# Optimization experiments

Measured on AMD Instinct MI355X. Metric: run time of the kernel, lower is better.

Reference implementation:

```python
import jax, jax.numpy as jnp
import numpy as np

N_NODES = 50000
N_EDGES = 800000
F_IN, F_HID, F_OUT = 128, 256, 64


def setup_inputs() -> dict:
    key = jax.random.key(0)
    ks = jax.random.split(key, 8)
    return {
        "x": jax.random.normal(ks[0], (N_NODES, F_IN), dtype=jnp.float32),
        "edge_index": jax.random.randint(ks[1], (2, N_EDGES), 0, N_NODES, dtype=jnp.int32),
        "W_l1": jax.random.normal(ks[2], (F_IN, F_HID), dtype=jnp.float32) * (1.0 / np.sqrt(F_IN)),
        "W_r1": jax.random.normal(ks[3], (F_IN, F_HID), dtype=jnp.float32) * (1.0 / np.sqrt(F_IN)),
        "b1": jnp.zeros((F_HID,), dtype=jnp.float32),
        "W_l2": jax.random.normal(ks[4], (F_HID, F_OUT), dtype=jnp.float32) * (1.0 / np.sqrt(F_HID)),
        "W_r2": jax.random.normal(ks[5], (F_HID, F_OUT), dtype=jnp.float32) * (1.0 / np.sqrt(F_HID)),
        "b2": jnp.zeros((F_OUT,), dtype=jnp.float32),
    }


def _sage_conv(x, src, dst, W_l, W_r, b):
    # PyG SAGEConv, mean aggregation:
    #   out = mean_{j in N(i)} x_j @ W_l + b + x_i @ W_r
    n = x.shape[0]
    msgs = x[src]                                              # [E, F] gather
    agg_sum = jax.ops.segment_sum(msgs, dst, num_segments=n)   # [N, F] scatter-add
    deg = jax.ops.segment_sum(jnp.ones_like(dst, dtype=x.dtype), dst, num_segments=n)
    agg = agg_sum / jnp.maximum(deg, 1.0)[:, None]             # isolated nodes -> 0
    return agg @ W_l + x @ W_r + b


def reference(x, edge_index, W_l1, W_r1, b1, W_l2, W_r2, b2):
    src, dst = edge_index[0], edge_index[1]
    # layer 1 + relu (dropout is identity in eval mode)
    h = jax.nn.relu(_sage_conv(x, src, dst, W_l1, W_r1, b1))
    # layer 2, multi_class=False -> sigmoid
    out = jax.nn.sigmoid(_sage_conv(h, src, dst, W_l2, W_r2, b2))
    return out
```

## Files before the change

### kernel.cpp

```cpp
#include <hip/hip_runtime.h>
#include <cstdint>
#include <cstddef>


#define N_NODES 50000
#define N_EDGES 800000
#define F_IN 128
#define F_HID 256
#define F_OUT 64
#define CAP 64

#define NBIN ((N_NODES + 255) / 256)
#define EPB 4096
#define NBLK_A ((N_EDGES + EPB - 1) / EPB)
#define CHUNK 64

#define PREP_TOTAL (N_NODES * 64 + 256 * 256 + 128 * 256)
#define NBLK_PREP ((PREP_TOTAL + 255) / 256)

typedef __attribute__((ext_vector_type(8))) short bf16x8;
typedef __attribute__((ext_vector_type(4))) float f32x4;
typedef __attribute__((ext_vector_type(2))) float f32x2;

__device__ inline unsigned short f2bf(float f) {
    unsigned int u = __float_as_uint(f);
    u += 0x7fffu + ((u >> 16) & 1u);
    return (unsigned short)(u >> 16);
}
__device__ inline unsigned int pack_bf2(float lo, float hi) {
    return (unsigned int)f2bf(lo) | ((unsigned int)f2bf(hi) << 16);
}
__device__ inline float bf_lo(unsigned int u) { return __uint_as_float(u << 16); }
__device__ inline float bf_hi(unsigned int u) { return __uint_as_float(u & 0xffff0000u); }

__global__ __launch_bounds__(256) void binprep_kernel(
    const int* __restrict__ src, const int* __restrict__ dst, int* __restrict__ blkbincnt,
    unsigned int* __restrict__ chunks, const float* __restrict__ x,
    const float* __restrict__ Wl1, const float* __restrict__ Wr1, const float* __restrict__ Wl2,
    const float* __restrict__ Wr2, unsigned int* __restrict__ xbf,
    unsigned short* __restrict__ xq16, short* __restrict__ Bt1, short* __restrict__ Bt2) {
    __shared__ unsigned int ls[NBIN * CHUNK];
    __shared__ int hist[NBIN];
    const int bid = blockIdx.x;
    const int tid = threadIdx.x;
    if (bid < NBLK_A) {
        for (int i = tid; i < NBIN; i += 256) hist[i] = 0;
        __syncthreads();
        const int base = bid * EPB;
        const int nloc = min(EPB, N_EDGES - base);
        for (int j = tid; j < nloc; j += 256) {
            int e = base + j;
            int d = dst[e];
            int s = src[e];
            int bin = d >> 8;
            int p = atomicAdd(&hist[bin], 1);
            if (p < CHUNK) ls[bin * CHUNK + p] = ((unsigned int)(d & 255) << 16) | (unsigned int)s;
        }
        __syncthreads();
        for (int i = tid; i < NBIN; i += 256) blkbincnt[bid * NBIN + i] = hist[i];
        unsigned int* outp = &chunks[(size_t)bid * NBIN * CHUNK];
        for (int idx = tid; idx < NBIN * CHUNK; idx += 256) {
            int bin = idx >> 6, i = idx & 63;
            if (i < min(hist[bin], CHUNK)) outp[idx] = ls[idx];
        }
        return;
    }
    int i = (bid - NBLK_A) * 256 + tid;
    if (i < N_NODES * 64) {
        int row = i >> 6, c = i & 63;
        float2 f = *reinterpret_cast<const float2*>(&x[(size_t)row * F_IN + 2 * c]);
        xbf[(size_t)row * 64 + c] = pack_bf2(f.x, f.y);
        xq16[(size_t)row * 64 + c] =
            (unsigned short)(__builtin_amdgcn_cvt_pk_fp8_f32(f.x, f.y, 0, false) & 0xffff);
        return;
    }
    i -= N_NODES * 64;
    if (i < 256 * 256) {
        int k = i >> 8, n = i & 255;
        float v = (k < 128) ? Wl1[k * 256 + n] : Wr1[(k - 128) * 256 + n];
        Bt1[n * 256 + k] = (short)f2bf(v);
        return;
    }
    i -= 256 * 256;
    if (i < 128 * 256) {
        int k = i >> 7, n = i & 127;
        float v = (n < 64) ? Wl2[k * 64 + n] : Wr2[k * 64 + (n - 64)];
        Bt2[n * 256 + k] = (short)f2bf(v);
    }
}

__global__ __launch_bounds__(256) void binpartB_kernel(const unsigned int* __restrict__ chunks,
                                                       const int* __restrict__ blkbincnt,
                                                       int* __restrict__ cnt,
                                                       unsigned short* __restrict__ slots) {
    __shared__ int cur[256];
    __shared__ unsigned short ls[256 * CAP];
    __shared__ int ccnt[NBLK_A];
    const int bin = blockIdx.x;
    const int tid = threadIdx.x;
    cur[tid] = 0;
    for (int i = tid; i < NBLK_A; i += 256) ccnt[i] = min(blkbincnt[i * NBIN + bin], CHUNK);
    __syncthreads();
    for (int idx = tid; idx < NBLK_A * CHUNK; idx += 256) {
        int blk = idx >> 6, i = idx & 63;
        if (i < ccnt[blk]) {
            unsigned int pk = chunks[((size_t)blk * NBIN + bin) * CHUNK + i];
            int dl = pk >> 16;
            int p = atomicAdd(&cur[dl], 1);
            if (p < CAP) ls[dl * CAP + p] = (unsigned short)(pk & 0xffffu);
        }
    }
    __syncthreads();
    const int node = bin * 256 + tid;
    if (node < N_NODES) cnt[node] = cur[tid];
    const uint4* lsv = reinterpret_cast<const uint4*>(ls);
    uint4* gv = reinterpret_cast<uint4*>(&slots[(size_t)bin * 256 * CAP]);
    for (int i = tid; i < 256 * 8; i += 256) {
        int row = i >> 3;
        if (bin * 256 + row < N_NODES) gv[i] = lsv[i];
    }
}

__global__ __launch_bounds__(256) void agg1_kernel(const unsigned int* __restrict__ xq,
                                                   unsigned int* __restrict__ aggx,
                                                   const int* __restrict__ cnt,
                                                   const unsigned short* __restrict__ slots) {
    const int node = blockIdx.x * 8 + (threadIdx.x >> 5);
    const int t = threadIdx.x & 31;
    if (node >= N_NODES) return;
    const int deg = cnt[node];
    const int n = min(deg, CAP);
    const unsigned short* sl = &slots[(size_t)node * CAP];
    float a0 = 0.f, a1 = 0.f, a2 = 0.f, a3 = 0.f;
    int j = 0;
    for (; j + 8 <= n; j += 8) {
        uint4 sv = *reinterpret_cast<const uint4*>(&sl[j]);
        int s[8];
        s[0] = sv.x & 0xffff; s[1] = sv.x >> 16;
        s[2] = sv.y & 0xffff; s[3] = sv.y >> 16;
        s[4] = sv.z & 0xffff; s[5] = sv.z >> 16;
        s[6] = sv.w & 0xffff; s[7] = sv.w >> 16;
        unsigned int u[8];
#pragma unroll
        for (int q = 0; q < 8; ++q) u[q] = xq[(size_t)s[q] * 32 + t];
#pragma unroll
        for (int q = 0; q < 8; ++q) {
            f32x2 lo = __builtin_amdgcn_cvt_pk_f32_fp8((int)u[q], false);
            f32x2 hi = __builtin_amdgcn_cvt_pk_f32_fp8((int)u[q], true);
            a0 += lo.x; a1 += lo.y; a2 += hi.x; a3 += hi.y;
        }
    }
    for (; j < n; ++j) {
        unsigned int u = xq[(size_t)sl[j] * 32 + t];
        f32x2 lo = __builtin_amdgcn_cvt_pk_f32_fp8((int)u, false);
        f32x2 hi = __builtin_amdgcn_cvt_pk_f32_fp8((int)u, true);
        a0 += lo.x; a1 += lo.y; a2 += hi.x; a3 += hi.y;
    }
    float scale = (deg > 0) ? 1.0f / (float)deg : 0.0f;
    uint2 o;
    o.x = pack_bf2(a0 * scale, a1 * scale);
    o.y = pack_bf2(a2 * scale, a3 * scale);
    *reinterpret_cast<uint2*>(&aggx[(size_t)node * 64 + t * 2]) = o;
}

#define LDK 72
#define LDH 264
__global__ __launch_bounds__(256) void gemm_fused_kernel(const short* __restrict__ Aagg,
                                                         const short* __restrict__ Aself,
                                                         const short* __restrict__ Bt1,
                                                         const short* __restrict__ Bt2,
                                                         const float* __restrict__ b1,
                                                         short* __restrict__ grL,
                                                         short* __restrict__ grR) {
    __shared__ short smem[64 * LDH + 128 * LDK];
    short* As = smem;
    short* Bs1 = smem + 64 * LDK;
    short* Hs = smem;
    short* Bs2 = smem + 64 * LDH;

    const int tid = threadIdx.x;
    const int lane = tid & 63;
    const int wave = tid >> 6;
    const int quad = lane >> 4;
    const int l16 = lane & 15;
    const int m0 = blockIdx.x * 64;
    const int M = N_NODES;

    f32x4 acc[4][4];
#pragma unroll
    for (int i = 0; i < 4; ++i)
#pragma unroll
        for (int j = 0; j < 4; ++j) acc[i][j] = (f32x4)(0.0f);

    const int wn1 = wave * 64;

    for (int k0 = 0; k0 < 256; k0 += 64) {
        const short* Asrc = (k0 < 128) ? Aagg : Aself;
        const int kbase = k0 & 127;
        for (int idx = tid; idx < 64 * 8; idx += 256) {
            int row = idx >> 3, seg = idx & 7;
            int gm = m0 + row;
            uint4 v = make_uint4(0, 0, 0, 0);
            if (gm < M)
                v = *reinterpret_cast<const uint4*>(&Asrc[(size_t)gm * 128 + kbase + seg * 8]);
            *reinterpret_cast<uint4*>(&As[row * LDK + seg * 8]) = v;
        }
        for (int idx = tid; idx < 256 * 8; idx += 256) {
            int row = idx >> 3, seg = idx & 7;
            uint4 v = *reinterpret_cast<const uint4*>(&Bt1[(size_t)row * 256 + k0 + seg * 8]);
            *reinterpret_cast<uint4*>(&Bs1[row * LDK + seg * 8]) = v;
        }
        __syncthreads();
#pragma unroll
        for (int kk = 0; kk < 64; kk += 32) {
            bf16x8 af[4], bfr[4];
#pragma unroll
            for (int mi = 0; mi < 4; ++mi)
                af[mi] = *reinterpret_cast<const bf16x8*>(
                    &As[(mi * 16 + l16) * LDK + kk + quad * 8]);
#pragma unroll
            for (int ni = 0; ni < 4; ++ni)
                bfr[ni] = *reinterpret_cast<const bf16x8*>(
                    &Bs1[(wn1 + ni * 16 + l16) * LDK + kk + quad * 8]);
#pragma unroll
            for (int mi = 0; mi < 4; ++mi)
#pragma unroll
                for (int ni = 0; ni < 4; ++ni)
                    acc[mi][ni] = __builtin_amdgcn_mfma_f32_16x16x32_bf16(af[mi], bfr[ni],
                                                                          acc[mi][ni], 0, 0, 0);
        }
        __syncthreads();
    }

    float biasv[4];
#pragma unroll
    for (int ni = 0; ni < 4; ++ni) biasv[ni] = b1[wn1 + ni * 16 + l16];
#pragma unroll
    for (int mi = 0; mi < 4; ++mi)
#pragma unroll
        for (int reg = 0; reg < 4; ++reg) {
            int row = mi * 16 + quad * 4 + reg;
#pragma unroll
            for (int ni = 0; ni < 4; ++ni) {
                float v = fmaxf(acc[mi][ni][reg] + biasv[ni], 0.0f);
                Hs[row * LDH + wn1 + ni * 16 + l16] = (short)f2bf(v);
            }
        }
    __syncthreads();

    f32x4 acc2[2][4];
#pragma unroll
    for (int i = 0; i < 2; ++i)
#pragma unroll
        for (int j = 0; j < 4; ++j) acc2[i][j] = (f32x4)(0.0f);

    const int wm2 = (wave >> 1) * 32;
    const int wn2 = (wave & 1) * 64;

    for (int k0 = 0; k0 < 256; k0 += 64) {
        for (int idx = tid; idx < 128 * 8; idx += 256) {
            int row = idx >> 3, seg = idx & 7;
            uint4 v = *reinterpret_cast<const uint4*>(&Bt2[(size_t)row * 256 + k0 + seg * 8]);
            *reinterpret_cast<uint4*>(&Bs2[row * LDK + seg * 8]) = v;
        }
        __syncthreads();
#pragma unroll
        for (int kk = 0; kk < 64; kk += 32) {
            bf16x8 af[2], bfr[4];
#pragma unroll
            for (int mi = 0; mi < 2; ++mi)
                af[mi] = *reinterpret_cast<const bf16x8*>(
                    &Hs[(wm2 + mi * 16 + l16) * LDH + k0 + kk + quad * 8]);
#pragma unroll
            for (int ni = 0; ni < 4; ++ni)
                bfr[ni] = *reinterpret_cast<const bf16x8*>(
                    &Bs2[(wn2 + ni * 16 + l16) * LDK + kk + quad * 8]);
#pragma unroll
            for (int mi = 0; mi < 2; ++mi)
#pragma unroll
                for (int ni = 0; ni < 4; ++ni)
                    acc2[mi][ni] = __builtin_amdgcn_mfma_f32_16x16x32_bf16(af[mi], bfr[ni],
                                                                           acc2[mi][ni], 0, 0, 0);
        }
        __syncthreads();
    }

#pragma unroll
    for (int mi = 0; mi < 2; ++mi)
#pragma unroll
        for (int reg = 0; reg < 4; ++reg) {
            int gm = m0 + wm2 + mi * 16 + quad * 4 + reg;
            if (gm >= M) continue;
#pragma unroll
            for (int ni = 0; ni < 4; ++ni) {
                int gn = wn2 + ni * 16 + l16;
                short o = (short)f2bf(acc2[mi][ni][reg]);
                if (gn < 64)
                    grL[(size_t)gm * 64 + gn] = o;
                else
                    grR[(size_t)gm * 64 + (gn - 64)] = o;
            }
        }
}

__global__ __launch_bounds__(256) void final_kernel(const unsigned int* __restrict__ grLu,
                                                    const unsigned int* __restrict__ grRu,
                                                    const int* __restrict__ cnt,
                                                    const unsigned short* __restrict__ slots,
                                                    const float* __restrict__ b2,
                                                    float* __restrict__ out) {
    const int node = blockIdx.x * 8 + (threadIdx.x >> 5);
    const int t = threadIdx.x & 31;
    if (node >= N_NODES) return;
    const int deg = cnt[node];
    const int n = min(deg, CAP);
    const unsigned short* sl = &slots[(size_t)node * CAP];
    float a0 = 0.f, a1 = 0.f;
    int j = 0;
    for (; j + 8 <= n; j += 8) {
        uint4 sv = *reinterpret_cast<const uint4*>(&sl[j]);
        int s[8];
        s[0] = sv.x & 0xffff; s[1] = sv.x >> 16;
        s[2] = sv.y & 0xffff; s[3] = sv.y >> 16;
        s[4] = sv.z & 0xffff; s[5] = sv.z >> 16;
        s[6] = sv.w & 0xffff; s[7] = sv.w >> 16;
        unsigned int u[8];
#pragma unroll
        for (int q = 0; q < 8; ++q) u[q] = grLu[(size_t)s[q] * 32 + t];
#pragma unroll
        for (int q = 0; q < 8; ++q) {
            a0 += bf_lo(u[q]);
            a1 += bf_hi(u[q]);
        }
    }
    for (; j < n; ++j) {
        unsigned int u = grLu[(size_t)sl[j] * 32 + t];
        a0 += bf_lo(u);
        a1 += bf_hi(u);
    }
    float scale = (deg > 0) ? 1.0f / (float)deg : 0.0f;
    unsigned int r = grRu[(size_t)node * 32 + t];
    float2 bv = *reinterpret_cast<const float2*>(&b2[t * 2]);
    float v0 = a0 * scale + bf_lo(r) + bv.x;
    float v1 = a1 * scale + bf_hi(r) + bv.y;
    float2 o;
    o.x = 1.0f / (1.0f + __expf(-v0));
    o.y = 1.0f / (1.0f + __expf(-v1));
    *reinterpret_cast<float2*>(&out[(size_t)node * 64 + t * 2]) = o;
}


extern "C" void kernel_launch(void* const* d_in, const int* in_sizes, int n_in,
                              void* d_out, int out_size, void* d_ws, size_t ws_size,
                              hipStream_t stream) {
    const float* x   = (const float*)d_in[0];
    const int* ei    = (const int*)d_in[1];
    const float* Wl1 = (const float*)d_in[2];
    const float* Wr1 = (const float*)d_in[3];
    const float* b1  = (const float*)d_in[4];
    const float* Wl2 = (const float*)d_in[5];
    const float* Wr2 = (const float*)d_in[6];
    const float* b2  = (const float*)d_in[7];
    float* out       = (float*)d_out;

    const int* src = ei;
    const int* dst = ei + N_EDGES;

    char* p = (char*)d_ws;
    auto alloc = [&](size_t bytes) {
        char* r = p;
        p += (bytes + 255) & ~(size_t)255;
        return (void*)r;
    };
    int* cnt              = (int*)alloc((size_t)N_NODES * 4);
    unsigned short* slots = (unsigned short*)alloc((size_t)NBIN * 256 * CAP * 2);
    int* blkbincnt        = (int*)alloc((size_t)NBLK_A * NBIN * 4);
    unsigned int* chunks  = (unsigned int*)alloc((size_t)NBLK_A * NBIN * CHUNK * 4);
    unsigned int* xbf     = (unsigned int*)alloc((size_t)N_NODES * 64 * 4);
    unsigned short* xq16  = (unsigned short*)alloc((size_t)N_NODES * 64 * 2);
    unsigned int* aggx    = (unsigned int*)alloc((size_t)N_NODES * 64 * 4);
    short* grL            = (short*)alloc((size_t)N_NODES * 64 * 2);
    short* grR            = (short*)alloc((size_t)N_NODES * 64 * 2);
    short* Bt1            = (short*)alloc((size_t)256 * 256 * 2);
    short* Bt2            = (short*)alloc((size_t)128 * 256 * 2);
    (void)ws_size;

    binprep_kernel<<<NBLK_A + NBLK_PREP, 256, 0, stream>>>(src, dst, blkbincnt, chunks, x, Wl1,
                                                           Wr1, Wl2, Wr2, xbf, xq16, Bt1, Bt2);
    binpartB_kernel<<<NBIN, 256, 0, stream>>>(chunks, blkbincnt, cnt, slots);

    agg1_kernel<<<(N_NODES + 7) / 8, 256, 0, stream>>>((const unsigned int*)xq16, aggx, cnt,
                                                       slots);

    gemm_fused_kernel<<<(N_NODES + 63) / 64, 256, 0, stream>>>(
        (const short*)aggx, (const short*)xbf, Bt1, Bt2, b1, grL, grR);

    final_kernel<<<(N_NODES + 7) / 8, 256, 0, stream>>>((const unsigned int*)grL,
                                                        (const unsigned int*)grR, cnt, slots, b2,
                                                        out);
}
```

Baseline: 203.2 us.

## Fuse bin partition with layer-1 neighbor aggregation using LDS slot lists

Merges the binning kernel and the first aggregation kernel into one 1024-thread block per 256-node bin. The aggregation reads neighbor lists and degrees straight from shared memory instead of re-reading slots and counts from global memory, and one kernel launch is removed. In exchange, only NBIN (~196) blocks run the gather-heavy aggregation, which may leave CUs underused and reduce the parallelism available to hide latency. The large LDS footprint also limits occupancy.

```diff
diff --git a/kernel.cpp b/kernel.cpp
--- a/kernel.cpp
+++ b/kernel.cpp
@@ -89,19 +89,21 @@
     }
 }
 
-__global__ __launch_bounds__(256) void binpartB_kernel(const unsigned int* __restrict__ chunks,
-                                                       const int* __restrict__ blkbincnt,
-                                                       int* __restrict__ cnt,
-                                                       unsigned short* __restrict__ slots) {
+__global__ __launch_bounds__(1024) void bpart_agg_kernel(const unsigned int* __restrict__ chunks,
+                                                         const int* __restrict__ blkbincnt,
+                                                         int* __restrict__ cnt,
+                                                         unsigned short* __restrict__ slots,
+                                                         const unsigned int* __restrict__ xq,
+                                                         unsigned int* __restrict__ aggx) {
     __shared__ int cur[256];
     __shared__ unsigned short ls[256 * CAP];
     __shared__ int ccnt[NBLK_A];
     const int bin = blockIdx.x;
     const int tid = threadIdx.x;
-    cur[tid] = 0;
-    for (int i = tid; i < NBLK_A; i += 256) ccnt[i] = min(blkbincnt[i * NBIN + bin], CHUNK);
+    if (tid < 256) cur[tid] = 0;
+    for (int i = tid; i < NBLK_A; i += 1024) ccnt[i] = min(blkbincnt[i * NBIN + bin], CHUNK);
     __syncthreads();
-    for (int idx = tid; idx < NBLK_A * CHUNK; idx += 256) {
+    for (int idx = tid; idx < NBLK_A * CHUNK; idx += 1024) {
         int blk = idx >> 6, i = idx & 63;
         if (i < ccnt[blk]) {
             unsigned int pk = chunks[((size_t)blk * NBIN + bin) * CHUNK + i];
@@ -111,56 +113,56 @@
         }
     }
     __syncthreads();
-    const int node = bin * 256 + tid;
-    if (node < N_NODES) cnt[node] = cur[tid];
+    if (tid < 256) {
+        int node = bin * 256 + tid;
+        if (node < N_NODES) cnt[node] = cur[tid];
+    }
     const uint4* lsv = reinterpret_cast<const uint4*>(ls);
     uint4* gv = reinterpret_cast<uint4*>(&slots[(size_t)bin * 256 * CAP]);
-    for (int i = tid; i < 256 * 8; i += 256) {
+    for (int i = tid; i < 256 * 8; i += 1024) {
         int row = i >> 3;
         if (bin * 256 + row < N_NODES) gv[i] = lsv[i];
     }
-}
-
-__global__ __launch_bounds__(256) void agg1_kernel(const unsigned int* __restrict__ xq,
-                                                   unsigned int* __restrict__ aggx,
-                                                   const int* __restrict__ cnt,
-                                                   const unsigned short* __restrict__ slots) {
-    const int node = blockIdx.x * 8 + (threadIdx.x >> 5);
-    const int t = threadIdx.x & 31;
-    if (node >= N_NODES) return;
-    const int deg = cnt[node];
-    const int n = min(deg, CAP);
-    const unsigned short* sl = &slots[(size_t)node * CAP];
-    float a0 = 0.f, a1 = 0.f, a2 = 0.f, a3 = 0.f;
-    int j = 0;
-    for (; j + 8 <= n; j += 8) {
-        uint4 sv = *reinterpret_cast<const uint4*>(&sl[j]);
-        int s[8];
-        s[0] = sv.x & 0xffff; s[1] = sv.x >> 16;
-        s[2] = sv.y & 0xffff; s[3] = sv.y >> 16;
-        s[4] = sv.z & 0xffff; s[5] = sv.z >> 16;
-        s[6] = sv.w & 0xffff; s[7] = sv.w >> 16;
-        unsigned int u[8];
-#pragma unroll
-        for (int q = 0; q < 8; ++q) u[q] = xq[(size_t)s[q] * 32 + t];
-#pragma unroll
-        for (int q = 0; q < 8; ++q) {
-            f32x2 lo = __builtin_amdgcn_cvt_pk_f32_fp8((int)u[q], false);
-            f32x2 hi = __builtin_amdgcn_cvt_pk_f32_fp8((int)u[q], true);
+    const int nl = tid >> 5;
+    const int t = tid & 31;
+    for (int nb = 0; nb < 8; ++nb) {
+        const int local = nb * 32 + nl;
+        const int node = bin * 256 + local;
+        if (node >= N_NODES) continue;
+        const int deg = cur[local];
+        const int n = min(deg, CAP);
+        const unsigned short* sl = &ls[local * CAP];
+        float a0 = 0.f, a1 = 0.f, a2 = 0.f, a3 = 0.f;
+        int j = 0;
+        for (; j + 8 <= n; j += 8) {
+            uint4 sv = *reinterpret_cast<const uint4*>(&sl[j]);
+            int s[8];
+            s[0] = sv.x & 0xffff; s[1] = sv.x >> 16;
+            s[2] = sv.y & 0xffff; s[3] = sv.y >> 16;
+            s[4] = sv.z & 0xffff; s[5] = sv.z >> 16;
+            s[6] = sv.w & 0xffff; s[7] = sv.w >> 16;
+            unsigned int u[8];
+#pragma unroll
+            for (int q = 0; q < 8; ++q) u[q] = xq[(size_t)s[q] * 32 + t];
+#pragma unroll
+            for (int q = 0; q < 8; ++q) {
+                f32x2 lo = __builtin_amdgcn_cvt_pk_f32_fp8((int)u[q], false);
+                f32x2 hi = __builtin_amdgcn_cvt_pk_f32_fp8((int)u[q], true);
+                a0 += lo.x; a1 += lo.y; a2 += hi.x; a3 += hi.y;
+            }
+        }
+        for (; j < n; ++j) {
+            unsigned int u = xq[(size_t)sl[j] * 32 + t];
+            f32x2 lo = __builtin_amdgcn_cvt_pk_f32_fp8((int)u, false);
+            f32x2 hi = __builtin_amdgcn_cvt_pk_f32_fp8((int)u, true);
             a0 += lo.x; a1 += lo.y; a2 += hi.x; a3 += hi.y;
         }
-    }
-    for (; j < n; ++j) {
-        unsigned int u = xq[(size_t)sl[j] * 32 + t];
-        f32x2 lo = __builtin_amdgcn_cvt_pk_f32_fp8((int)u, false);
-        f32x2 hi = __builtin_amdgcn_cvt_pk_f32_fp8((int)u, true);
-        a0 += lo.x; a1 += lo.y; a2 += hi.x; a3 += hi.y;
-    }
-    float scale = (deg > 0) ? 1.0f / (float)deg : 0.0f;
-    uint2 o;
-    o.x = pack_bf2(a0 * scale, a1 * scale);
-    o.y = pack_bf2(a2 * scale, a3 * scale);
-    *reinterpret_cast<uint2*>(&aggx[(size_t)node * 64 + t * 2]) = o;
+        float scale = (deg > 0) ? 1.0f / (float)deg : 0.0f;
+        uint2 o;
+        o.x = pack_bf2(a0 * scale, a1 * scale);
+        o.y = pack_bf2(a2 * scale, a3 * scale);
+        *reinterpret_cast<uint2*>(&aggx[(size_t)node * 64 + t * 2]) = o;
+    }
 }
 
 #define LDK 72
@@ -387,10 +389,8 @@
 
     binprep_kernel<<<NBLK_A + NBLK_PREP, 256, 0, stream>>>(src, dst, blkbincnt, chunks, x, Wl1,
                                                            Wr1, Wl2, Wr2, xbf, xq16, Bt1, Bt2);
-    binpartB_kernel<<<NBIN, 256, 0, stream>>>(chunks, blkbincnt, cnt, slots);
-
-    agg1_kernel<<<(N_NODES + 7) / 8, 256, 0, stream>>>((const unsigned int*)xq16, aggx, cnt,
-                                                       slots);
+    bpart_agg_kernel<<<NBIN, 1024, 0, stream>>>(chunks, blkbincnt, cnt, slots,
+                                                (const unsigned int*)xq16, aggx);
 
     gemm_fused_kernel<<<(N_NODES + 63) / 64, 256, 0, stream>>>(
         (const short*)aggx, (const short*)xbf, Bt1, Bt2, b1, grL, grR);
```

After: 193.9 us. 4.6% less time.
